# Kernel optimization log

Hardware: AMD Instinct MI355X
Metric: run time of the kernel (lower is better)

Reference implementation:

```python
import jax, jax.numpy as jnp
import numpy as np

EPS = 1e-5  # BatchNorm eps (eval mode, running_mean=0, running_var=1)


def conv1x1(x, w):
    # x: [n,c,h,w], w: [o,c]
    return jnp.einsum('nchw,oc->nohw', x, w)


def bn_relu(x, s, b):
    scale = s / jnp.sqrt(1.0 + EPS)
    return jax.nn.relu(x * scale[None, :, None, None] + b[None, :, None, None])


def upsample_bilinear_ac(x, out_h, out_w):
    # nn.Upsample(mode='bilinear', align_corners=True)
    n, c, h, w = x.shape
    ys = jnp.linspace(0.0, h - 1.0, out_h)
    xs = jnp.linspace(0.0, w - 1.0, out_w)
    y0 = jnp.floor(ys).astype(jnp.int32)
    y1 = jnp.minimum(y0 + 1, h - 1)
    x0 = jnp.floor(xs).astype(jnp.int32)
    x1 = jnp.minimum(x0 + 1, w - 1)
    wy = (ys - y0)[None, None, :, None]
    wx = (xs - x0)[None, None, None, :]
    rows = x[:, :, y0, :] * (1.0 - wy) + x[:, :, y1, :] * wy
    return rows[:, :, :, x0] * (1.0 - wx) + rows[:, :, :, x1] * wx


def to_patches(x, ph, pw):
    # [n,c,H,W] -> [n,c,P,L], P = (H//ph)*(W//pw) patches, L = ph*pw pixels
    n, c, H, W = x.shape
    gh, gw = H // ph, W // pw
    return x.reshape(n, c, gh, ph, gw, pw).transpose(0, 1, 2, 4, 3, 5).reshape(n, c, gh * gw, ph * pw)


def from_patches(x, H, W, ph, pw):
    n, c, P, L = x.shape
    gh, gw = H // ph, W // pw
    return x.reshape(n, c, gh, gw, ph, pw).transpose(0, 1, 2, 4, 3, 5).reshape(n, c, H, W)


def patch_attention(q, k, v, ph, pw, H, W):
    qp = to_patches(q, ph, pw)
    kp = to_patches(k, ph, pw)
    vp = to_patches(v, ph, pw)
    # patch-vs-patch similarity, contracted over pixels within a patch
    sim = jax.nn.sigmoid(jnp.einsum('ncpl,ncql->ncpq', qp, kp))
    # sim1 (mean over key patches) + sim2 (mean over query patches), both [n,c,P,1]
    gate = sim.mean(axis=3, keepdims=True) + sim.mean(axis=2)[..., None]
    return from_patches(gate * vp, H, W, ph, pw)


def setup_inputs() -> dict:
    key = jax.random.key(0)
    ks = jax.random.split(key, 20)
    N, Ch, Cl, neck = 8, 256, 512, 64
    H = W = 128
    Hs = Ws = 32
    sc = 0.05
    return {
        'branch0_feats': jax.random.normal(ks[0], (N, Ch, H, W), jnp.float32),
        'other_feats': jax.random.normal(ks[1], (N, Cl, Hs, Ws), jnp.float32),
        'wq1': jax.random.normal(ks[2], (neck, Ch), jnp.float32) * sc,
        'bnq1_s': jax.random.uniform(ks[3], (neck,), jnp.float32, 0.5, 1.5),
        'bnq1_b': jax.random.normal(ks[4], (neck,), jnp.float32) * 0.1,
        'wk1': jax.random.normal(ks[5], (neck, Cl), jnp.float32) * sc,
        'bnk1_s': jax.random.uniform(ks[6], (neck,), jnp.float32, 0.5, 1.5),
        'bnk1_b': jax.random.normal(ks[7], (neck,), jnp.float32) * 0.1,
        'wv1': jax.random.normal(ks[8], (neck, Ch), jnp.float32) * sc,
        'wq2': jax.random.normal(ks[9], (neck, Ch), jnp.float32) * sc,
        'bnq2_s': jax.random.uniform(ks[10], (neck,), jnp.float32, 0.5, 1.5),
        'bnq2_b': jax.random.normal(ks[11], (neck,), jnp.float32) * 0.1,
        'wk2': jax.random.normal(ks[12], (neck, Cl), jnp.float32) * sc,
        'bnk2_s': jax.random.uniform(ks[13], (neck,), jnp.float32, 0.5, 1.5),
        'bnk2_b': jax.random.normal(ks[14], (neck,), jnp.float32) * 0.1,
        'wz': jax.random.normal(ks[15], (Ch, 2 * neck), jnp.float32) * sc,
        'alpha': jax.random.uniform(ks[16], (1,), jnp.float32),
        'gamma': jax.random.uniform(ks[17], (1,), jnp.float32),
    }


def reference(branch0_feats, other_feats, wq1, bnq1_s, bnq1_b, wk1, bnk1_s, bnk1_b, wv1,
              wq2, bnq2_s, bnq2_b, wk2, bnk2_s, bnk2_b, wz, alpha, gamma):
    _, _, H, W = branch0_feats.shape
    _, _, Hs, Ws = other_feats.shape

    value = conv1x1(branch0_feats, wv1)
    query = bn_relu(conv1x1(branch0_feats, wq1), bnq1_s, bnq1_b)
    key = upsample_bilinear_ac(bn_relu(conv1x1(other_feats, wk1), bnk1_s, bnk1_b), H, W)

    half = query.shape[1] // 2
    # scale 1: patches of size (Hs, Ws)
    ctx0 = patch_attention(query[:, :half], key[:, :half], value[:, :half], Hs, Ws, H, W)
    # scale 2: patches of size (Hs//2, Ws//2)
    ctx2 = patch_attention(query[:, half:], key[:, half:], value[:, half:], Hs // 2, Ws // 2, H, W)

    # dense per-pixel sigmoid gating branch
    query2 = bn_relu(conv1x1(branch0_feats, wq2), bnq2_s, bnq2_b)
    key2 = upsample_bilinear_ac(bn_relu(conv1x1(other_feats, wk2), bnk2_s, bnk2_b), H, W)
    ctx3 = value * jax.nn.sigmoid(query2 * key2)

    context = jnp.concatenate([alpha[0] * jnp.concatenate([ctx0, ctx2], axis=1),
                               gamma[0] * ctx3], axis=1)
    return conv1x1(context, wz)
```

## Files before the change

### kernel.cpp

```cpp
#include <hip/hip_runtime.h>
#include <hip/hip_bf16.h>
#include <math.h>
#include <stdint.h>

#define N_    8
#define CH    256
#define CL    512
#define NECK  64
#define H_    128
#define W_    128
#define HW    16384
#define HWS   1024
#define EPSB  1e-5f
#define SC31  (31.0f/127.0f)

typedef unsigned short ushort_t;
typedef __attribute__((ext_vector_type(8))) short bf16x8;
typedef __attribute__((ext_vector_type(4))) float f32x4;

union bfpack  { ushort_t u[8]; bf16x8 v; };
union bfpack4 { uint32_t u[4]; bf16x8 v; };

__device__ __forceinline__ float sigmoidf_(float x){ return 1.0f/(1.0f + __expf(-x)); }

__device__ __forceinline__ ushort_t f2bf(float x){
    union { __hip_bfloat16 h; ushort_t u; } cv;
    cv.h = __float2bfloat16(x);
    return cv.u;
}
__device__ __forceinline__ uint32_t pack2(float lo, float hi){
    return (uint32_t)f2bf(lo) | ((uint32_t)f2bf(hi) << 16);
}
__device__ __forceinline__ float bf2f(ushort_t b){
    union { uint32_t u; float f; } v; v.u = ((uint32_t)b) << 16;
    return v.f;
}

__global__ __launch_bounds__(512, 4) void k_phase1(
    const float* __restrict__ x,
    const float* __restrict__ xo,
    const float* __restrict__ wv1, const float* __restrict__ wq1, const float* __restrict__ wq2,
    const float* __restrict__ wk1, const float* __restrict__ wk2,
    const float* __restrict__ s1, const float* __restrict__ b1,
    const float* __restrict__ s2, const float* __restrict__ b2,
    const float* __restrict__ sk1, const float* __restrict__ bk1,
    const float* __restrict__ sk2, const float* __restrict__ bk2,
    const float* __restrict__ wz,
    ushort_t* __restrict__ value, ushort_t* __restrict__ query, ushort_t* __restrict__ query2,
    float* __restrict__ k1s, float* __restrict__ k2s, ushort_t* __restrict__ Wzb)
{
    __shared__ __align__(16) char smem[65536];
    int blk = blockIdx.x;
    int t = threadIdx.x;
    int lane = t & 63, w8 = t >> 6;
    int r16 = lane & 15;
    float inv = rsqrtf(1.0f + EPSB);

    if (blk < 64){
        ushort_t* At = (ushort_t*)smem;
        ushort_t* Bt = (ushort_t*)(smem + 16384);
        int wm = w8 >> 1, wn = w8 & 1;
        int b = blk;
        int n = b >> 3, pix0 = (b & 7) << 7;
        f32x4 acc[2][4];
        #pragma unroll
        for (int m=0;m<2;m++)
            #pragma unroll
            for (int nn=0;nn<4;nn++) acc[m][nn] = (f32x4){0.f,0.f,0.f,0.f};

        const float* xb = xo + (size_t)n*CL*HWS + pix0;
        float va[8], vb[8];
        {
            const float* xc = xb + (size_t)(8*w8)*HWS;
            #pragma unroll
            for (int j=0;j<8;j++){
                va[j] = xc[(size_t)j*HWS + lane];
                vb[j] = xc[(size_t)j*HWS + 64 + lane];
            }
        }
        int oo = t >> 3, c8 = t & 7;
        for (int kt=0; kt<8; ++kt){
            int c0 = kt*64;
            const float* ws0 = wk1 + (size_t)oo*CL + c0 + c8*8;
            const float* ws1 = wk2 + (size_t)oo*CL + c0 + c8*8;
            float4 a00 = *(const float4*)ws0, a01 = *(const float4*)(ws0+4);
            float4 a10 = *(const float4*)ws1, a11 = *(const float4*)(ws1+4);
            uint32_t pa[4], pb[4];
            #pragma unroll
            for (int j=0;j<4;j++){
                pa[j] = pack2(va[2*j], va[2*j+1]);
                pb[j] = pack2(vb[2*j], vb[2*j+1]);
            }
            int offA = (lane*128 + w8*16) ^ ((lane&7)<<4);
            int offB = ((lane+64)*128 + w8*16) ^ ((lane&7)<<4);
            *(uint4*)((char*)Bt + offA) = make_uint4(pa[0],pa[1],pa[2],pa[3]);
            *(uint4*)((char*)Bt + offB) = make_uint4(pb[0],pb[1],pb[2],pb[3]);
            {
                int off0 = (oo*128 + c8*16) ^ ((oo&7)<<4);
                int off1 = ((64+oo)*128 + c8*16) ^ ((oo&7)<<4);
                *(uint4*)((char*)At + off0) = make_uint4(pack2(a00.x,a00.y),pack2(a00.z,a00.w),
                                                         pack2(a01.x,a01.y),pack2(a01.z,a01.w));
                *(uint4*)((char*)At + off1) = make_uint4(pack2(a10.x,a10.y),pack2(a10.z,a10.w),
                                                         pack2(a11.x,a11.y),pack2(a11.z,a11.w));
            }
            __syncthreads();
            if (kt < 7){
                const float* xc = xb + (size_t)((kt+1)*64 + 8*w8)*HWS;
                #pragma unroll
                for (int j=0;j<8;j++){
                    va[j] = xc[(size_t)j*HWS + lane];
                    vb[j] = xc[(size_t)j*HWS + 64 + lane];
                }
            }
            #pragma unroll
            for (int ks=0; ks<2; ++ks){
                bf16x8 a[2], bfr[4];
                #pragma unroll
                for (int m=0;m<2;m++){
                    int row = wm*32 + m*16 + r16;
                    int off = (row*128 + ks*64 + (lane>>4)*16) ^ ((row&7)<<4);
                    a[m] = *(const bf16x8*)((const char*)At + off);
                }
                #pragma unroll
                for (int nn=0;nn<4;nn++){
                    int row = wn*64 + nn*16 + r16;
                    int off = (row*128 + ks*64 + (lane>>4)*16) ^ ((row&7)<<4);
                    bfr[nn] = *(const bf16x8*)((const char*)Bt + off);
                }
                #pragma unroll
                for (int m=0;m<2;m++)
                    #pragma unroll
                    for (int nn=0;nn<4;nn++)
                        acc[m][nn] = __builtin_amdgcn_mfma_f32_16x16x32_bf16(a[m], bfr[nn], acc[m][nn], 0, 0, 0);
            }
            __syncthreads();
        }
        #pragma unroll
        for (int m=0;m<2;m++){
            int obase = wm*32 + m*16 + ((lane>>4)<<2);
            #pragma unroll
            for (int r=0;r<4;r++){
                int o = obase + r;
                int oc = o & 63;
                float sc = ((o<64) ? sk1[oc] : sk2[oc]) * inv;
                float bb =  (o<64) ? bk1[oc] : bk2[oc];
                float* dst = ((o<64) ? k1s : k2s) + ((size_t)n*NECK + oc)*HWS + pix0;
                #pragma unroll
                for (int nn=0;nn<4;nn++){
                    int px = wn*64 + nn*16 + r16;
                    dst[px] = fmaxf(fmaf(acc[m][nn][r], sc, bb), 0.f);
                }
            }
        }
        return;
    }

    if (blk < 80){
        int i = (blk - 64)*2048 + t*4;
        float4 f = *(const float4*)(wz + i);
        *(uint2*)(Wzb + i) = make_uint2(pack2(f.x,f.y), pack2(f.z,f.w));
        return;
    }

    ushort_t* Bt = (ushort_t*)smem;
    int tile = blk - 80;
    int n = tile >> 7;
    int pix0 = (tile & 127) << 7;
    int wm = w8 >> 1, wn = w8 & 1;

    {
        int px = t & 127, chg = t >> 7;
        const float* xc = x + (size_t)n*CH*HW + (size_t)(chg*64)*HW + pix0 + px;
        #pragma unroll
        for (int pass=0; pass<4; ++pass){
            float v[16];
            #pragma unroll
            for (int j=0;j<16;j++) v[j] = xc[(size_t)(pass*16 + j)*HW];
            uint32_t p[8];
            #pragma unroll
            for (int j=0;j<8;j++) p[j] = pack2(v[2*j], v[2*j+1]);
            int base = px*512 + chg*128 + pass*32;
            int o0 = base ^ ((px&7)<<4);
            int o1 = (base + 16) ^ ((px&7)<<4);
            *(uint4*)((char*)Bt + o0) = make_uint4(p[0],p[1],p[2],p[3]);
            *(uint4*)((char*)Bt + o1) = make_uint4(p[4],p[5],p[6],p[7]);
        }
    }
    __syncthreads();

    f32x4 acc[3][4];
    #pragma unroll
    for (int m=0;m<3;m++)
        #pragma unroll
        for (int nn=0;nn<4;nn++) acc[m][nn] = (f32x4){0.f,0.f,0.f,0.f};

    const float* abase[3];
    #pragma unroll
    for (int m=0;m<3;m++){
        int row = wm*48 + m*16 + r16;
        const float* wsrc = (row < 64)  ? (wv1 + (size_t)row*CH)
                          : (row < 128) ? (wq1 + (size_t)(row-64)*CH)
                                        : (wq2 + (size_t)(row-128)*CH);
        abase[m] = wsrc + (lane>>4)*8;
    }

    #pragma unroll
    for (int ks=0; ks<8; ++ks){
        bf16x8 a[3], b[4];
        #pragma unroll
        for (int m=0;m<3;m++){
            const float* s = abase[m] + ks*32;
            float4 f0 = *(const float4*)s, f1 = *(const float4*)(s+4);
            bfpack4 pk;
            pk.u[0] = pack2(f0.x,f0.y); pk.u[1] = pack2(f0.z,f0.w);
            pk.u[2] = pack2(f1.x,f1.y); pk.u[3] = pack2(f1.z,f1.w);
            a[m] = pk.v;
        }
        #pragma unroll
        for (int nn=0;nn<4;nn++){
            int row = wn*64 + nn*16 + r16;
            int off = (row*512 + ks*64 + (lane>>4)*16) ^ ((row&7)<<4);
            b[nn] = *(const bf16x8*)((const char*)Bt + off);
        }
        #pragma unroll
        for (int m=0;m<3;m++)
            #pragma unroll
            for (int nn=0;nn<4;nn++)
                acc[m][nn] = __builtin_amdgcn_mfma_f32_16x16x32_bf16(a[m], b[nn], acc[m][nn], 0, 0, 0);
    }

    #pragma unroll
    for (int m=0;m<3;m++){
        int obase = wm*48 + m*16 + ((lane>>4)<<2);
        #pragma unroll
        for (int r=0;r<4;r++){
            int o = obase + r;
            int grp = o >> 6, oc = o & 63;
            float sc = 1.f, bb = 0.f;
            ushort_t* dst;
            if (grp == 0) dst = value;
            else if (grp == 1){ sc = s1[oc]*inv; bb = b1[oc]; dst = query; }
            else              { sc = s2[oc]*inv; bb = b2[oc]; dst = query2; }
            #pragma unroll
            for (int nn=0;nn<4;nn++){
                int pix = pix0 + wn*64 + nn*16 + r16;
                float v = acc[m][nn][r];
                if (grp) v = fmaxf(fmaf(v, sc, bb), 0.f);
                dst[((size_t)(n*NECK + oc))*HW + pix] = f2bf(v);
            }
        }
    }
}

__global__ __launch_bounds__(256) void k_gates(
    const ushort_t* __restrict__ query, const float* __restrict__ k1small,
    float* __restrict__ gate1, float* __restrict__ gate2)
{
    __shared__ __align__(16) char smem[69632];
    int bid = blockIdx.x;
    int t = threadIdx.x;
    int lane = t & 63, wv = t >> 6;
    int r16 = lane & 15, g = lane >> 4;
    float* ksm = (float*)smem;
    ushort_t* qt = (ushort_t*)(smem + 4096);
    ushort_t* kt = (ushort_t*)(smem + 4096 + 32768);

    if (bid < 256){
        int n = bid >> 5, c = bid & 31;
        const float* ks = k1small + (size_t)(n*NECK + c)*HWS;
        #pragma unroll
        for (int i=0;i<4;i++) ksm[i*256+t] = ks[i*256+t];
        __syncthreads();
        const ushort_t* qb = query + (size_t)(n*NECK + c)*HW;
        #pragma unroll
        for (int i=0;i<8;i++){
            int task = i*256 + t;
            int p = task >> 7, c8 = task & 127;
            int ly = c8 >> 2, lx8 = (c8 & 3)*8;
            int h = (p>>2)*32 + ly, w = (p&3)*32 + lx8;
            bf16x8 qv = *(const bf16x8*)(qb + h*W_ + w);
            int off = (p*2048 + c8*16) ^ ((p&7)<<4);
            *(bf16x8*)((char*)qt + off) = qv;
            float yf = h*SC31; int y0=(int)yf; int y1=min(y0+1,31); float fy=yf-(float)y0;
            bfpack pk;
            #pragma unroll
            for (int j=0;j<8;j++){
                int ww = w + j;
                float xf = ww*SC31; int x0=(int)xf; int x1=min(x0+1,31); float fx=xf-(float)x0;
                float a=ksm[y0*32+x0], b=ksm[y0*32+x1], cc=ksm[y1*32+x0], d=ksm[y1*32+x1];
                float r0=a+(b-a)*fx, r1=cc+(d-cc)*fx;
                pk.u[j] = f2bf(r0 + (r1-r0)*fy);
            }
            *(bf16x8*)((char*)kt + off) = pk.v;
        }
        __syncthreads();
        f32x4 acc = (f32x4){0.f,0.f,0.f,0.f};
        #pragma unroll
        for (int k8=0; k8<8; ++k8){
            int l0 = wv*256 + k8*32 + g*8;
            int off = (r16*2048 + l0*2) ^ ((r16&7)<<4);
            bf16x8 av = *(const bf16x8*)((char*)qt + off);
            bf16x8 bv = *(const bf16x8*)((char*)kt + off);
            acc = __builtin_amdgcn_mfma_f32_16x16x32_bf16(av, bv, acc, 0, 0, 0);
        }
        __syncthreads();
        float* pw = (float*)smem;
        #pragma unroll
        for (int r=0;r<4;r++)
            pw[wv*256 + (g*4+r)*16 + r16] = acc[r];
        __syncthreads();
        float* simM = (float*)(smem + 4096);
        float s = pw[t] + pw[256+t] + pw[512+t] + pw[768+t];
        simM[t] = sigmoidf_(s);
        __syncthreads();
        if (t < 16){
            float rs=0.f, cs=0.f;
            #pragma unroll
            for (int q=0;q<16;q++) rs += simM[t*16+q];
            #pragma unroll
            for (int p=0;p<16;p++) cs += simM[p*16+t];
            gate1[(size_t)(n*32 + c)*16 + t] = (rs + cs) * (1.0f/16.0f);
        }
    } else {
        int b2 = bid - 256;
        int n = b2 >> 5, cl = b2 & 31, c = 32 + cl;
        const float* ks = k1small + (size_t)(n*NECK + c)*HWS;
        #pragma unroll
        for (int i=0;i<4;i++) ksm[i*256+t] = ks[i*256+t];
        __syncthreads();
        const ushort_t* qb = query + (size_t)(n*NECK + c)*HW;
        #pragma unroll
        for (int i=0;i<8;i++){
            int task = i*256 + t;
            int p = task >> 5, c8 = task & 31;
            int ly = c8 >> 1, lx8 = (c8 & 1)*8;
            int h = (p>>3)*16 + ly, w = (p&7)*16 + lx8;
            bf16x8 qv = *(const bf16x8*)(qb + h*W_ + w);
            int off = (p*512 + c8*16) ^ ((p&7)<<4);
            *(bf16x8*)((char*)qt + off) = qv;
            float yf = h*SC31; int y0=(int)yf; int y1=min(y0+1,31); float fy=yf-(float)y0;
            bfpack pk;
            #pragma unroll
            for (int j=0;j<8;j++){
                int ww = w + j;
                float xf = ww*SC31; int x0=(int)xf; int x1=min(x0+1,31); float fx=xf-(float)x0;
                float a=ksm[y0*32+x0], b=ksm[y0*32+x1], cc=ksm[y1*32+x0], d=ksm[y1*32+x1];
                float r0=a+(b-a)*fx, r1=cc+(d-cc)*fx;
                pk.u[j] = f2bf(r0 + (r1-r0)*fy);
            }
            *(bf16x8*)((char*)kt + off) = pk.v;
        }
        __syncthreads();
        f32x4 acc2[4];
        #pragma unroll
        for (int qc=0;qc<4;qc++) acc2[qc] = (f32x4){0.f,0.f,0.f,0.f};
        #pragma unroll
        for (int k8=0; k8<8; ++k8){
            int l0 = k8*32 + g*8;
            int offA = ((wv*16 + r16)*512 + l0*2) ^ ((r16&7)<<4);
            bf16x8 av = *(const bf16x8*)((char*)qt + offA);
            #pragma unroll
            for (int qc=0;qc<4;qc++){
                int offB = ((qc*16 + r16)*512 + l0*2) ^ ((r16&7)<<4);
                bf16x8 bv = *(const bf16x8*)((char*)kt + offB);
                acc2[qc] = __builtin_amdgcn_mfma_f32_16x16x32_bf16(av, bv, acc2[qc], 0, 0, 0);
            }
        }
        __syncthreads();
        float* simM = (float*)smem;
        #pragma unroll
        for (int qc=0;qc<4;qc++)
            #pragma unroll
            for (int r=0;r<4;r++){
                int p = wv*16 + g*4 + r, q = qc*16 + r16;
                simM[p*65 + q] = sigmoidf_(acc2[qc][r]);
            }
        __syncthreads();
        if (t < 64){
            float rs=0.f, cs=0.f;
            for (int q=0;q<64;q++) rs += simM[t*65 + q];
            for (int p=0;p<64;p++) cs += simM[p*65 + t];
            gate2[(size_t)(n*32 + cl)*64 + t] = (rs + cs) * (1.0f/64.0f);
        }
    }
}

__global__ __launch_bounds__(512, 4) void k_final_mfma(
    const ushort_t* __restrict__ value, const ushort_t* __restrict__ query2,
    const float* __restrict__ k2small,
    const float* __restrict__ gate1, const float* __restrict__ gate2,
    const ushort_t* __restrict__ Wzb,
    const float* __restrict__ alpha_p, const float* __restrict__ gamma_p,
    float* __restrict__ out)
{
    __shared__ __align__(16) char smem[59392];
    ushort_t* Ct = (ushort_t*)smem;
    float* g1s = (float*)(smem + 32768);
    float* g2s = (float*)(smem + 34816);
    float* k2r = (float*)(smem + 43008);
    int blk = blockIdx.x;
    int n = blk >> 7, h = blk & 127;
    int pix0 = h << 7;
    int t = threadIdx.x;
    int lane = t & 63;
    int wid = t >> 6;
    int wm = wid >> 1, wn = wid & 1;

    int px = t & 127, qd = t >> 7;
    const size_t vbase = (size_t)n*NECK*HW + pix0 + px;
    ushort_t vreg[16], qreg[16];
    #pragma unroll
    for (int i=0;i<16;i++){
        int c = qd*16 + i;
        vreg[i] = value [vbase + (size_t)c*HW];
        qreg[i] = query2[vbase + (size_t)c*HW];
    }

    float alpha = alpha_p[0], gamma = gamma_p[0];
    g1s[t & 511] = gate1[(size_t)n*512 + (t & 511)];
    #pragma unroll
    for (int i=0;i<4;i++) g2s[i*512 + t] = gate2[(size_t)n*2048 + i*512 + t];

    float yf = h * SC31;
    int y0 = (int)yf, y1 = min(y0+1, 31);
    float fy = yf - (float)y0;
    #pragma unroll
    for (int i=0;i<8;i++){
        int e = i*512 + t;
        int buf = e >> 11, c = (e >> 5) & 63, xx = e & 31;
        k2r[buf*2048 + c*32 + xx] = k2small[((size_t)n*NECK + c)*HWS + (buf ? y1 : y0)*32 + xx];
    }
    __syncthreads();

    float xf = px * SC31;
    int x0 = (int)xf, x1 = min(x0+1, 31);
    float fx = xf - (float)x0;
    int patch1 = (h>>5)*4 + (px>>5);
    int patch2 = (h>>4)*8 + (px>>4);
    #pragma unroll
    for (int j=0;j<2;j++){
        bfpack pk;
        #pragma unroll
        for (int i=0;i<8;i++){
            int ch = qd*16 + j*8 + i;
            float g = (ch < 32) ? g1s[ch*16 + patch1] : g2s[(ch-32)*64 + patch2];
            pk.u[i] = f2bf(alpha * g * bf2f(vreg[j*8+i]));
        }
        int off = (px*256 + qd*32 + j*16) ^ ((px&7)<<4);
        *(bf16x8*)((char*)Ct + off) = pk.v;
    }
    #pragma unroll
    for (int j=0;j<2;j++){
        bfpack pk;
        #pragma unroll
        for (int i=0;i<8;i++){
            int c = qd*16 + j*8 + i;
            float vv = bf2f(vreg[j*8+i]);
            float q2 = bf2f(qreg[j*8+i]);
            float r0 = k2r[c*32+x0];      r0 += (k2r[c*32+x1] - r0)*fx;
            float r1 = k2r[2048+c*32+x0]; r1 += (k2r[2048+c*32+x1] - r1)*fx;
            float kv = r0 + (r1 - r0)*fy;
            pk.u[i] = f2bf(gamma * vv * sigmoidf_(q2*kv));
        }
        int off = (px*256 + 128 + qd*32 + j*16) ^ ((px&7)<<4);
        *(bf16x8*)((char*)Ct + off) = pk.v;
    }
    __syncthreads();

    f32x4 acc[4][4];
    #pragma unroll
    for (int m=0;m<4;m++)
        #pragma unroll
        for (int nn=0;nn<4;nn++) acc[m][nn] = (f32x4){0.f,0.f,0.f,0.f};
    #pragma unroll
    for (int ks=0; ks<4; ++ks){
        bf16x8 a[4], b[4];
        #pragma unroll
        for (int m=0;m<4;m++){
            int row = wm*64 + m*16 + (lane&15);
            a[m] = *(const bf16x8*)(Wzb + row*128 + ks*32 + (lane>>4)*8);
        }
        #pragma unroll
        for (int nn=0;nn<4;nn++){
            int row = wn*64 + nn*16 + (lane&15);
            int off = (row*256 + ks*64 + (lane>>4)*16) ^ ((row&7)<<4);
            b[nn] = *(const bf16x8*)((const char*)Ct + off);
        }
        #pragma unroll
        for (int m=0;m<4;m++)
            #pragma unroll
            for (int nn=0;nn<4;nn++)
                acc[m][nn] = __builtin_amdgcn_mfma_f32_16x16x32_bf16(a[m], b[nn], acc[m][nn], 0, 0, 0);
    }

    #pragma unroll
    for (int m=0;m<4;m++){
        int obase = wm*64 + m*16 + ((lane>>4)<<2);
        #pragma unroll
        for (int r=0;r<4;r++){
            int o = obase + r;
            float* dst = out + ((size_t)(n*CH + o))*HW + pix0 + wn*64 + (lane&15);
            #pragma unroll
            for (int nn=0;nn<4;nn++)
                dst[nn*16] = acc[m][nn][r];
        }
    }
}

extern "C" void kernel_launch(void* const* d_in, const int* in_sizes, int n_in,
                              void* d_out, int out_size, void* d_ws, size_t ws_size,
                              hipStream_t stream) {
    const float* x0  = (const float*)d_in[0];
    const float* xo  = (const float*)d_in[1];
    const float* wq1 = (const float*)d_in[2];
    const float* s1  = (const float*)d_in[3];
    const float* b1  = (const float*)d_in[4];
    const float* wk1 = (const float*)d_in[5];
    const float* sk1 = (const float*)d_in[6];
    const float* bk1 = (const float*)d_in[7];
    const float* wv1 = (const float*)d_in[8];
    const float* wq2 = (const float*)d_in[9];
    const float* s2  = (const float*)d_in[10];
    const float* b2  = (const float*)d_in[11];
    const float* wk2 = (const float*)d_in[12];
    const float* sk2 = (const float*)d_in[13];
    const float* bk2 = (const float*)d_in[14];
    const float* wz  = (const float*)d_in[15];
    const float* alp = (const float*)d_in[16];
    const float* gam = (const float*)d_in[17];

    ushort_t* value  = (ushort_t*)d_ws;
    ushort_t* query  = value  + 8388608;
    ushort_t* query2 = query  + 8388608;
    float*    k1s    = (float*)(query2 + 8388608);
    float*    k2s    = k1s + 524288;
    float*    g1     = k2s + 524288;
    float*    g2     = g1 + 4096;
    ushort_t* Wzb    = (ushort_t*)(g2 + 16384);

    k_phase1<<<dim3(1104), dim3(512), 0, stream>>>(
        x0, xo, wv1, wq1, wq2, wk1, wk2, s1, b1, s2, b2, sk1, bk1, sk2, bk2, wz,
        value, query, query2, k1s, k2s, Wzb);
    k_gates<<<dim3(512), dim3(256), 0, stream>>>(query, k1s, g1, g2);
    k_final_mfma<<<dim3(1024), dim3(512), 0, stream>>>(value, query2, k2s, g1, g2, Wzb,
                                                       alp, gam, (float*)d_out);
}
```

Measured before the change: 145.7 us.

## Split phase1 into transpose-to-bf16 stage and LDS-staged big GEMM kernel

The fp32 input is first transposed into a channel-last bf16 buffer (reusing the output buffer as scratch) and the fused 1x1 weights are pre-converted to bf16. A separate GEMM kernel then streams both operands into LDS with direct global-to-LDS loads in swizzled 64-channel chunks. This replaces strided per-pixel fp32 loads and per-iteration weight conversion in registers. In exchange it adds an extra kernel launch and a full round trip of the transposed activation through global memory.

Result: faster. 137.9 us (-5.3%).

```diff
diff --git a/kernel.cpp b/kernel.cpp
--- a/kernel.cpp
+++ b/kernel.cpp
@@ -19,7 +19,6 @@
 typedef __attribute__((ext_vector_type(4))) float f32x4;
 
 union bfpack  { ushort_t u[8]; bf16x8 v; };
-union bfpack4 { uint32_t u[4]; bf16x8 v; };
 
 __device__ __forceinline__ float sigmoidf_(float x){ return 1.0f/(1.0f + __expf(-x)); }
 
@@ -36,31 +35,80 @@
     return v.f;
 }
 
-__global__ __launch_bounds__(512, 4) void k_phase1(
-    const float* __restrict__ x,
-    const float* __restrict__ xo,
+__device__ __forceinline__ void gload16(const void* g, void* l){
+    __builtin_amdgcn_global_load_lds((const __attribute__((address_space(1))) void*)g,
+                                     (__attribute__((address_space(3))) void*)l, 16, 0, 0);
+}
+
+__global__ __launch_bounds__(512) void k_stage(
+    const float* __restrict__ x, const float* __restrict__ xo,
     const float* __restrict__ wv1, const float* __restrict__ wq1, const float* __restrict__ wq2,
     const float* __restrict__ wk1, const float* __restrict__ wk2,
-    const float* __restrict__ s1, const float* __restrict__ b1,
-    const float* __restrict__ s2, const float* __restrict__ b2,
     const float* __restrict__ sk1, const float* __restrict__ bk1,
     const float* __restrict__ sk2, const float* __restrict__ bk2,
     const float* __restrict__ wz,
-    ushort_t* __restrict__ value, ushort_t* __restrict__ query, ushort_t* __restrict__ query2,
-    float* __restrict__ k1s, float* __restrict__ k2s, ushort_t* __restrict__ Wzb)
+    ushort_t* __restrict__ XT,
+    float* __restrict__ k1s, float* __restrict__ k2s,
+    ushort_t* __restrict__ Wzb, ushort_t* __restrict__ Wbig)
 {
-    __shared__ __align__(16) char smem[65536];
+    __shared__ __align__(16) char smem[33280];
     int blk = blockIdx.x;
     int t = threadIdx.x;
-    int lane = t & 63, w8 = t >> 6;
-    int r16 = lane & 15;
-    float inv = rsqrtf(1.0f + EPSB);
-
-    if (blk < 64){
+
+    if (blk < 2048){
+        ushort_t* tile = (ushort_t*)smem;
+        int n = blk >> 8;
+        int r = blk & 255;
+        int cb = (r >> 6) << 6;
+        int pb = (r & 63) << 8;
+        const float* s = x + ((size_t)n*CH + cb)*HW + pb;
+        int cl = t >> 6, p4 = (t & 63)*4;
+        #pragma unroll
+        for (int i=0;i<8;i++){
+            int c = i*8 + cl;
+            float4 f = *(const float4*)(s + (size_t)c*HW + p4);
+            *(uint2*)&tile[c*260 + p4] = make_uint2(pack2(f.x,f.y), pack2(f.z,f.w));
+        }
+        __syncthreads();
+        int p = t >> 1, half = t & 1, c2 = half*32;
+        ushort_t* d = XT + ((size_t)n*HW + pb + p)*CH + cb + c2;
+        uint32_t w[16];
+        #pragma unroll
+        for (int j=0;j<16;j++){
+            int c = c2 + 2*j;
+            w[j] = (uint32_t)tile[c*260 + p] | ((uint32_t)tile[(c+1)*260 + p] << 16);
+        }
+        #pragma unroll
+        for (int k=0;k<4;k++)
+            *(uint4*)(d + 8*k) = make_uint4(w[4*k],w[4*k+1],w[4*k+2],w[4*k+3]);
+        return;
+    }
+
+    if (blk >= 2128){
+        int e = (blk - 2128)*2048 + t*4;
+        int o = e >> 8, c = e & 255;
+        const float* w = (o < 64) ? (wv1 + (size_t)o*CH)
+                       : (o < 128) ? (wq1 + (size_t)(o-64)*CH)
+                                   : (wq2 + (size_t)(o-128)*CH);
+        float4 f = *(const float4*)(w + c);
+        *(uint2*)(Wbig + e) = make_uint2(pack2(f.x,f.y), pack2(f.z,f.w));
+        return;
+    }
+    if (blk >= 2112){
+        int i = (blk - 2112)*2048 + t*4;
+        float4 f = *(const float4*)(wz + i);
+        *(uint2*)(Wzb + i) = make_uint2(pack2(f.x,f.y), pack2(f.z,f.w));
+        return;
+    }
+
+    {
         ushort_t* At = (ushort_t*)smem;
         ushort_t* Bt = (ushort_t*)(smem + 16384);
+        int lane = t & 63, w8 = t >> 6;
         int wm = w8 >> 1, wn = w8 & 1;
-        int b = blk;
+        int r16 = lane & 15;
+        float inv = rsqrtf(1.0f + EPSB);
+        int b = blk - 2048;
         int n = b >> 3, pix0 = (b & 7) << 7;
         f32x4 acc[2][4];
         #pragma unroll
@@ -152,41 +200,24 @@
                 }
             }
         }
-        return;
-    }
-
-    if (blk < 80){
-        int i = (blk - 64)*2048 + t*4;
-        float4 f = *(const float4*)(wz + i);
-        *(uint2*)(Wzb + i) = make_uint2(pack2(f.x,f.y), pack2(f.z,f.w));
-        return;
-    }
-
-    ushort_t* Bt = (ushort_t*)smem;
-    int tile = blk - 80;
-    int n = tile >> 7;
-    int pix0 = (tile & 127) << 7;
-    int wm = w8 >> 1, wn = w8 & 1;
-
-    {
-        int px = t & 127, chg = t >> 7;
-        const float* xc = x + (size_t)n*CH*HW + (size_t)(chg*64)*HW + pix0 + px;
-        #pragma unroll
-        for (int pass=0; pass<4; ++pass){
-            float v[16];
-            #pragma unroll
-            for (int j=0;j<16;j++) v[j] = xc[(size_t)(pass*16 + j)*HW];
-            uint32_t p[8];
-            #pragma unroll
-            for (int j=0;j<8;j++) p[j] = pack2(v[2*j], v[2*j+1]);
-            int base = px*512 + chg*128 + pass*32;
-            int o0 = base ^ ((px&7)<<4);
-            int o1 = (base + 16) ^ ((px&7)<<4);
-            *(uint4*)((char*)Bt + o0) = make_uint4(p[0],p[1],p[2],p[3]);
-            *(uint4*)((char*)Bt + o1) = make_uint4(p[4],p[5],p[6],p[7]);
-        }
-    }
-    __syncthreads();
+    }
+}
+
+__global__ __launch_bounds__(512) void k_gemm_big(
+    const ushort_t* __restrict__ XT,
+    const ushort_t* __restrict__ Wb,
+    const float* __restrict__ s1, const float* __restrict__ b1,
+    const float* __restrict__ s2, const float* __restrict__ b2,
+    ushort_t* __restrict__ value, ushort_t* __restrict__ query, ushort_t* __restrict__ query2)
+{
+    __shared__ ushort_t At[192*64];
+    __shared__ ushort_t Bt[128*64];
+    int blk = blockIdx.x;
+    int n = blk >> 7;
+    int pix0 = (blk & 127) << 7;
+    int t = threadIdx.x;
+    int wid = t >> 6, lane = t & 63;
+    int wm = wid >> 1, wn = wid & 1;
 
     f32x4 acc[3][4];
     #pragma unroll
@@ -194,41 +225,46 @@
         #pragma unroll
         for (int nn=0;nn<4;nn++) acc[m][nn] = (f32x4){0.f,0.f,0.f,0.f};
 
-    const float* abase[3];
-    #pragma unroll
-    for (int m=0;m<3;m++){
-        int row = wm*48 + m*16 + r16;
-        const float* wsrc = (row < 64)  ? (wv1 + (size_t)row*CH)
-                          : (row < 128) ? (wq1 + (size_t)(row-64)*CH)
-                                        : (wq2 + (size_t)(row-128)*CH);
-        abase[m] = wsrc + (lane>>4)*8;
-    }
-
-    #pragma unroll
-    for (int ks=0; ks<8; ++ks){
-        bf16x8 a[3], b[4];
-        #pragma unroll
-        for (int m=0;m<3;m++){
-            const float* s = abase[m] + ks*32;
-            float4 f0 = *(const float4*)s, f1 = *(const float4*)(s+4);
-            bfpack4 pk;
-            pk.u[0] = pack2(f0.x,f0.y); pk.u[1] = pack2(f0.z,f0.w);
-            pk.u[2] = pack2(f1.x,f1.y); pk.u[3] = pack2(f1.z,f1.w);
-            a[m] = pk.v;
-        }
-        #pragma unroll
-        for (int nn=0;nn<4;nn++){
-            int row = wn*64 + nn*16 + r16;
-            int off = (row*512 + ks*64 + (lane>>4)*16) ^ ((row&7)<<4);
-            b[nn] = *(const bf16x8*)((const char*)Bt + off);
-        }
-        #pragma unroll
-        for (int m=0;m<3;m++)
-            #pragma unroll
-            for (int nn=0;nn<4;nn++)
-                acc[m][nn] = __builtin_amdgcn_mfma_f32_16x16x32_bf16(a[m], b[nn], acc[m][nn], 0, 0, 0);
-    }
-
+    const ushort_t* Xb = XT + ((size_t)n*HW + pix0)*CH;
+    for (int kt=0; kt<4; ++kt){
+        int c0 = kt*64;
+        #pragma unroll
+        for (int i=0;i<3;i++){
+            int g = i*512 + t;
+            int s = g ^ ((g>>3)&7);
+            gload16(Wb + (size_t)(s>>3)*CH + c0 + (s&7)*8, (char*)At + g*16);
+        }
+        #pragma unroll
+        for (int i=0;i<2;i++){
+            int g = i*512 + t;
+            int s = g ^ ((g>>3)&7);
+            gload16(Xb + (size_t)(s>>3)*CH + c0 + (s&7)*8, (char*)Bt + g*16);
+        }
+        __syncthreads();
+        #pragma unroll
+        for (int ks=0; ks<2; ++ks){
+            bf16x8 a[3], b[4];
+            #pragma unroll
+            for (int m=0;m<3;m++){
+                int row = wm*48 + m*16 + (lane&15);
+                int off = (row*128 + ks*64 + (lane>>4)*16) ^ ((row&7)<<4);
+                a[m] = *(const bf16x8*)((const char*)At + off);
+            }
+            #pragma unroll
+            for (int nn=0;nn<4;nn++){
+                int row = wn*64 + nn*16 + (lane&15);
+                int off = (row*128 + ks*64 + (lane>>4)*16) ^ ((row&7)<<4);
+                b[nn] = *(const bf16x8*)((const char*)Bt + off);
+            }
+            #pragma unroll
+            for (int m=0;m<3;m++)
+                #pragma unroll
+                for (int nn=0;nn<4;nn++)
+                    acc[m][nn] = __builtin_amdgcn_mfma_f32_16x16x32_bf16(a[m], b[nn], acc[m][nn], 0, 0, 0);
+        }
+        __syncthreads();
+    }
+    float inv = rsqrtf(1.0f + EPSB);
     #pragma unroll
     for (int m=0;m<3;m++){
         int obase = wm*48 + m*16 + ((lane>>4)<<2);
@@ -243,7 +279,7 @@
             else              { sc = s2[oc]*inv; bb = b2[oc]; dst = query2; }
             #pragma unroll
             for (int nn=0;nn<4;nn++){
-                int pix = pix0 + wn*64 + nn*16 + r16;
+                int pix = pix0 + wn*64 + nn*16 + (lane&15);
                 float v = acc[m][nn][r];
                 if (grp) v = fmaxf(fmaf(v, sc, bb), 0.f);
                 dst[((size_t)(n*NECK + oc))*HW + pix] = f2bf(v);
@@ -537,10 +573,14 @@
     float*    g1     = k2s + 524288;
     float*    g2     = g1 + 4096;
     ushort_t* Wzb    = (ushort_t*)(g2 + 16384);
-
-    k_phase1<<<dim3(1104), dim3(512), 0, stream>>>(
-        x0, xo, wv1, wq1, wq2, wk1, wk2, s1, b1, s2, b2, sk1, bk1, sk2, bk2, wz,
-        value, query, query2, k1s, k2s, Wzb);
+    ushort_t* Wbig   = Wzb + 32768;
+    ushort_t* XT     = (ushort_t*)d_out;
+
+    k_stage<<<dim3(2152), dim3(512), 0, stream>>>(
+        x0, xo, wv1, wq1, wq2, wk1, wk2, sk1, bk1, sk2, bk2, wz,
+        XT, k1s, k2s, Wzb, Wbig);
+    k_gemm_big<<<dim3(1024), dim3(512), 0, stream>>>(
+        XT, Wbig, s1, b1, s2, b2, value, query, query2);
     k_gates<<<dim3(512), dim3(256), 0, stream>>>(query, k1s, g1, g2);
     k_final_mfma<<<dim3(1024), dim3(512), 0, stream>>>(value, query2, k2s, g1, g2, Wzb,
                                                        alp, gam, (float*)d_out);
```
